# Kernel tuning notes

Measured on AMD Instinct MI355X. Metric: run time of the kernel, lower is better.

The kernel has to match this reference:

```python
import jax, jax.numpy as jnp
import numpy as np

HIDDEN = 4096
INTER = 11008
B, S = 8, 16
QMAX = 127  # int8 symmetric range for w_bits=8


def setup_inputs() -> dict:
    key = jax.random.key(0)
    ks = jax.random.split(key, 7)
    hidden_state = jax.random.normal(ks[0], (B, S, HIDDEN), dtype=jnp.float32)
    # Quantized weights stored as integer values in float32 (as the dequant source)
    w1_q = jax.random.randint(ks[1], (INTER, HIDDEN), -QMAX - 1, QMAX + 1).astype(jnp.float32)
    w3_q = jax.random.randint(ks[2], (INTER, HIDDEN), -QMAX - 1, QMAX + 1).astype(jnp.float32)
    w2_q = jax.random.randint(ks[3], (HIDDEN, INTER), -QMAX - 1, QMAX + 1).astype(jnp.float32)
    # Per-output-channel dequant scales (has_scale=True)
    w1_s = jax.random.uniform(ks[4], (INTER,), dtype=jnp.float32, minval=0.5, maxval=1.5) * 0.01
    w3_s = jax.random.uniform(ks[5], (INTER,), dtype=jnp.float32, minval=0.5, maxval=1.5) * 0.01
    w2_s = jax.random.uniform(ks[6], (HIDDEN,), dtype=jnp.float32, minval=0.5, maxval=1.5) * 0.01
    return {"hidden_state": hidden_state, "w1_q": w1_q, "w1_s": w1_s,
            "w3_q": w3_q, "w3_s": w3_s, "w2_q": w2_q, "w2_s": w2_s}


def _dequant_linear(x, w_q, w_s):
    # w_q: [out, in] integer-valued weights; w_s: [out] per-channel scale
    # y = x @ (w_q * w_s[:, None]).T == (x @ w_q.T) * w_s
    return jnp.einsum('bsh,oh->bso', x, w_q) * w_s


def reference(hidden_state, w1_q, w1_s, w3_q, w3_s, w2_q, w2_s):
    up = _dequant_linear(hidden_state, w1_q, w1_s)      # [B,S,INTER]
    gate = _dequant_linear(hidden_state, w3_q, w3_s)    # [B,S,INTER]
    h = jax.nn.silu(up) * gate                          # SwiGLU
    return _dequant_linear(h, w2_q, w2_s)               # [B,S,HIDDEN]
```

## Files before the change

kernel.cpp:

```cpp
#include <hip/hip_runtime.h>

#define HIDDEN 4096
#define INTER  11008
#define MTOK   128
#define NMERG  (2*INTER)
#define KS1    4
#define KS2    16

typedef short          short8  __attribute__((ext_vector_type(8)));
typedef unsigned short ushort8 __attribute__((ext_vector_type(8)));
typedef float          f32x16  __attribute__((ext_vector_type(16)));
#define AS1 __attribute__((address_space(1)))
#define AS3 __attribute__((address_space(3)))

static __device__ __forceinline__ unsigned short f2bf_rne(float f) {
    unsigned u = __builtin_bit_cast(unsigned, f);
    u += 0x7FFFu + ((u >> 16) & 1u);
    return (unsigned short)(u >> 16);
}
static __device__ __forceinline__ float bf2f(unsigned short b) {
    unsigned u = (unsigned)b << 16;
    return __builtin_bit_cast(float, u);
}
static __device__ __forceinline__ int pk2(float lo, float hi) {
    return (int)__builtin_amdgcn_perm(__builtin_bit_cast(unsigned, hi),
                                      __builtin_bit_cast(unsigned, lo),
                                      0x07060302u);
}

__global__ void cvt_x_k(const float* __restrict__ x, unsigned short* __restrict__ A2) {
    int f = blockIdx.x * 256 + threadIdx.x;
    int lane = f & 63, w = f >> 6;
    int kstep = w >> 2, ms = w & 3;
    int m = ms * 32 + (lane & 31);
    int k = kstep * 16 + (lane >> 5) * 8;
    const float* src = x + (size_t)m * HIDDEN + k;
    float4 v0 = *(const float4*)(src);
    float4 v1 = *(const float4*)(src + 4);
    ushort8 o;
    o[0] = f2bf_rne(v0.x); o[1] = f2bf_rne(v0.y); o[2] = f2bf_rne(v0.z); o[3] = f2bf_rne(v0.w);
    o[4] = f2bf_rne(v1.x); o[5] = f2bf_rne(v1.y); o[6] = f2bf_rne(v1.z); o[7] = f2bf_rne(v1.w);
    *(ushort8*)(A2 + (size_t)f * 8) = o;
}

template<bool OBF16>
__global__ __launch_bounds__(256) void gemm_k(
    const unsigned short* __restrict__ A2,
    const float* __restrict__ B0, const float* __restrict__ B1, int nhalf,
    void* __restrict__ part, int K, int N, int totTiles, int ksplit)
{
    __shared__ __align__(16) float lds[16384];
    const int lane = threadIdx.x & 63;
    const int ws   = threadIdx.x >> 6;
    const int n0   = blockIdx.x * 128;
    const int ks   = blockIdx.y;
    const int tbeg = (ks * totTiles) / ksplit;
    const int tend = ((ks + 1) * totTiles) / ksplit;
    const int nt   = tend - tbeg;

    const char* gbase[8];
#pragma unroll
    for (int i = 0; i < 8; ++i) {
        int s = ws * 512 + i * 64 + lane;
        int n = s >> 4;
        int a = (s & 15) ^ (n & 15);
        const float* rowp = (n0 + n < nhalf) ? (B0 + (size_t)(n0 + n) * K)
                                             : (B1 + (size_t)(n0 + n - nhalf) * K);
        gbase[i] = (const char*)rowp + a * 16;
    }

    f32x16 acc[4];
#pragma unroll
    for (int t = 0; t < 4; ++t)
#pragma unroll
        for (int r = 0; r < 16; ++r) acc[t][r] = 0.f;

    const int nl = ws * 32 + (lane & 31);

    auto stage = [&](int t, int buf) {
        const size_t koff = (size_t)t * 64 * 4;
#pragma unroll
        for (int i = 0; i < 8; ++i) {
            __builtin_amdgcn_global_load_lds(
                (const AS1 unsigned*)(gbase[i] + koff),
                (AS3 unsigned*)((char*)lds + buf * 32768 + ws * 8192 + i * 1024), 16, 0, 0);
        }
    };
    auto loadA = [&](int t, short8 (&Ar)[16]) {
#pragma unroll
        for (int r = 0; r < 16; ++r) {
            int kg = t * 4 + (r >> 2), ms = r & 3;
            Ar[r] = *(const short8*)(A2 + ((size_t)(kg * 4 + ms) * 64 + lane) * 8);
        }
    };

    short8 A0[16], A1[16];

    auto iter = [&](int i, short8 (&Ar)[16]) {
        if (i + 1 < nt) { asm volatile("s_waitcnt vmcnt(24)" ::: "memory"); }
        else            { asm volatile("s_waitcnt vmcnt(0)" ::: "memory"); }
        __builtin_amdgcn_sched_barrier(0);

        const char* lbase = (const char*)lds + (size_t)(i & 1) * 32768;
#pragma unroll
        for (int step = 0; step < 4; ++step) {
            int a0 = step * 4 + ((lane >> 5) << 1);
            int p0 = nl * 16 + (a0 ^ (nl & 15));
            int p1 = nl * 16 + ((a0 + 1) ^ (nl & 15));
            float4 v0 = *(const float4*)(lbase + p0 * 16);
            float4 v1 = *(const float4*)(lbase + p1 * 16);
            int4 bi;
            bi.x = pk2(v0.x, v0.y); bi.y = pk2(v0.z, v0.w);
            bi.z = pk2(v1.x, v1.y); bi.w = pk2(v1.z, v1.w);
            short8 bf = __builtin_bit_cast(short8, bi);
#pragma unroll
            for (int ms = 0; ms < 4; ++ms)
                acc[ms] = __builtin_amdgcn_mfma_f32_32x32x16_bf16(Ar[step * 4 + ms], bf, acc[ms], 0, 0, 0);
        }

        if (i + 2 < nt) {
            asm volatile("s_waitcnt lgkmcnt(0)" ::: "memory");
            __builtin_amdgcn_sched_barrier(0);
            stage(tbeg + i + 2, i & 1);
            loadA(tbeg + i + 2, Ar);
        }
    };

    stage(tbeg, 0);
    loadA(tbeg, A0);
    if (nt > 1) { stage(tbeg + 1, 1); loadA(tbeg + 1, A1); }

    for (int i = 0; i < nt; i += 2) {
        iter(i, A0);
        if (i + 1 < nt) iter(i + 1, A1);
    }

    const int n = n0 + ws * 32 + (lane & 31);
#pragma unroll
    for (int ms = 0; ms < 4; ++ms)
#pragma unroll
        for (int r = 0; r < 16; ++r) {
            int m = ms * 32 + (r & 3) + 8 * (r >> 2) + 4 * (lane >> 5);
            size_t idx = ((size_t)ks * MTOK + m) * (size_t)N + n;
            if (OBF16) ((unsigned short*)part)[idx] = f2bf_rne(acc[ms][r]);
            else       ((float*)part)[idx] = acc[ms][r];
        }
}

__global__ void swiglu_k(const unsigned short* __restrict__ p1,
                         const float* __restrict__ s1, const float* __restrict__ s3,
                         unsigned short* __restrict__ h2)
{
    int f = blockIdx.x * 256 + threadIdx.x;
    int lane = f & 63, w = f >> 6;
    int kstep = w >> 2, ms = w & 3;
    int m = ms * 32 + (lane & 31);
    int j = kstep * 16 + (lane >> 5) * 8;
    float up[8], gt[8];
#pragma unroll
    for (int e = 0; e < 8; ++e) { up[e] = 0.f; gt[e] = 0.f; }
#pragma unroll
    for (int ks = 0; ks < KS1; ++ks) {
        const unsigned short* pu = p1 + ((size_t)ks * MTOK + m) * NMERG + j;
        ushort8 u = *(const ushort8*)(pu);
        ushort8 g = *(const ushort8*)(pu + INTER);
#pragma unroll
        for (int e = 0; e < 8; ++e) { up[e] += bf2f(u[e]); gt[e] += bf2f(g[e]); }
    }
    float4 c1a = *(const float4*)(s1 + j), c1b = *(const float4*)(s1 + j + 4);
    float4 c3a = *(const float4*)(s3 + j), c3b = *(const float4*)(s3 + j + 4);
    float c1[8] = {c1a.x, c1a.y, c1a.z, c1a.w, c1b.x, c1b.y, c1b.z, c1b.w};
    float c3[8] = {c3a.x, c3a.y, c3a.z, c3a.w, c3b.x, c3b.y, c3b.z, c3b.w};
    ushort8 o;
#pragma unroll
    for (int e = 0; e < 8; ++e) {
        float u = up[e] * c1[e], g = gt[e] * c3[e];
        o[e] = f2bf_rne(g * u / (1.f + __expf(-u)));
    }
    *(ushort8*)(h2 + (size_t)f * 8) = o;
}

__global__ void reduce_k(const float* __restrict__ p, const float* __restrict__ s2,
                         float* __restrict__ out)
{
    int i = (blockIdx.x * 256 + threadIdx.x) * 4;
    float4 acc = *(const float4*)(p + i);
#pragma unroll
    for (int s = 1; s < KS2; ++s) {
        float4 v = *(const float4*)(p + (size_t)s * MTOK * HIDDEN + i);
        acc.x += v.x; acc.y += v.y; acc.z += v.z; acc.w += v.w;
    }
    int ncol = i & (HIDDEN - 1);
    float4 sc = *(const float4*)(s2 + ncol);
    acc.x *= sc.x; acc.y *= sc.y; acc.z *= sc.z; acc.w *= sc.w;
    *(float4*)(out + i) = acc;
}

extern "C" void kernel_launch(void* const* d_in, const int* in_sizes, int n_in,
                              void* d_out, int out_size, void* d_ws, size_t ws_size,
                              hipStream_t stream) {
    const float* x   = (const float*)d_in[0];
    const float* w1q = (const float*)d_in[1];
    const float* w1s = (const float*)d_in[2];
    const float* w3q = (const float*)d_in[3];
    const float* w3s = (const float*)d_in[4];
    const float* w2q = (const float*)d_in[5];
    const float* w2s = (const float*)d_in[6];
    float* out = (float*)d_out;

    char* ws = (char*)d_ws;
    unsigned short* xb2 = (unsigned short*)ws;
    unsigned short* h2  = (unsigned short*)(ws + (1u << 20));
    void* part          = (void*)(ws + (4u << 20));

    cvt_x_k<<<MTOK * HIDDEN / 8 / 256, 256, 0, stream>>>(x, xb2);
    gemm_k<true><<<dim3(NMERG / 128, KS1), 256, 0, stream>>>(
        xb2, w1q, w3q, INTER, part, HIDDEN, NMERG, HIDDEN / 64, KS1);
    swiglu_k<<<MTOK * INTER / 8 / 256, 256, 0, stream>>>(
        (const unsigned short*)part, w1s, w3s, h2);
    gemm_k<false><<<dim3(HIDDEN / 128, KS2), 256, 0, stream>>>(
        h2, w2q, w2q, 1 << 30, part, INTER, HIDDEN, INTER / 64, KS2);
    reduce_k<<<MTOK * HIDDEN / 4 / 256, 256, 0, stream>>>(
        (const float*)part, w2s, out);
}
```

Before: 528.9 us.

## Retile GEMM to 32-column N tiles with 256-deep K stages and less split-K

Shrinks each block's output tile from 128 to 32 weight rows, with each wave owning one 32-token M slice instead of an N slice. Each stage now loads 256 K values per row into padded LDS rows. Split-K drops from 4/16 to 1/4, so there are far fewer partial-sum writes and reads while the grid grows in N. Block-wide barriers are added around LDS reuse. The cost is that each B fragment now feeds only one MFMA per wave, and the K loop per block is longer.

```diff
diff --git a/kernel.cpp b/kernel.cpp
--- a/kernel.cpp
+++ b/kernel.cpp
@@ -4,8 +4,11 @@
 #define INTER  11008
 #define MTOK   128
 #define NMERG  (2*INTER)
-#define KS1    4
-#define KS2    16
+#define KS1    1
+#define KS2    4
+#define SK     256
+#define RST    1040
+#define TILE   (32*RST)
 
 typedef short          short8  __attribute__((ext_vector_type(8)));
 typedef unsigned short ushort8 __attribute__((ext_vector_type(8)));
@@ -49,102 +52,88 @@
     const float* __restrict__ B0, const float* __restrict__ B1, int nhalf,
     void* __restrict__ part, int K, int N, int totTiles, int ksplit)
 {
-    __shared__ __align__(16) float lds[16384];
+    __shared__ __align__(16) char lds[2 * TILE];
     const int lane = threadIdx.x & 63;
     const int ws   = threadIdx.x >> 6;
-    const int n0   = blockIdx.x * 128;
+    const int n0   = blockIdx.x * 32;
     const int ks   = blockIdx.y;
     const int tbeg = (ks * totTiles) / ksplit;
     const int tend = ((ks + 1) * totTiles) / ksplit;
     const int nt   = tend - tbeg;
 
-    const char* gbase[8];
-#pragma unroll
-    for (int i = 0; i < 8; ++i) {
-        int s = ws * 512 + i * 64 + lane;
-        int n = s >> 4;
-        int a = (s & 15) ^ (n & 15);
-        const float* rowp = (n0 + n < nhalf) ? (B0 + (size_t)(n0 + n) * K)
-                                             : (B1 + (size_t)(n0 + n - nhalf) * K);
-        gbase[i] = (const char*)rowp + a * 16;
-    }
-
-    f32x16 acc[4];
-#pragma unroll
-    for (int t = 0; t < 4; ++t)
-#pragma unroll
-        for (int r = 0; r < 16; ++r) acc[t][r] = 0.f;
-
-    const int nl = ws * 32 + (lane & 31);
+    const char* rowp[8];
+#pragma unroll
+    for (int r = 0; r < 8; ++r) {
+        int n = n0 + ws * 8 + r;
+        const float* p = (n < nhalf) ? B0 + (size_t)n * K
+                                     : B1 + (size_t)(n - nhalf) * K;
+        rowp[r] = (const char*)p + lane * 16;
+    }
+
+    f32x16 acc;
+#pragma unroll
+    for (int r = 0; r < 16; ++r) acc[r] = 0.f;
 
     auto stage = [&](int t, int buf) {
-        const size_t koff = (size_t)t * 64 * 4;
-#pragma unroll
-        for (int i = 0; i < 8; ++i) {
+        const size_t koff = (size_t)t * (SK * 4);
+#pragma unroll
+        for (int r = 0; r < 8; ++r) {
             __builtin_amdgcn_global_load_lds(
-                (const AS1 unsigned*)(gbase[i] + koff),
-                (AS3 unsigned*)((char*)lds + buf * 32768 + ws * 8192 + i * 1024), 16, 0, 0);
+                (const AS1 unsigned*)(rowp[r] + koff),
+                (AS3 unsigned*)(lds + buf * TILE + (ws * 8 + r) * RST), 16, 0, 0);
         }
     };
     auto loadA = [&](int t, short8 (&Ar)[16]) {
 #pragma unroll
-        for (int r = 0; r < 16; ++r) {
-            int kg = t * 4 + (r >> 2), ms = r & 3;
-            Ar[r] = *(const short8*)(A2 + ((size_t)(kg * 4 + ms) * 64 + lane) * 8);
+        for (int s = 0; s < 16; ++s) {
+            int kg = t * 16 + s;
+            Ar[s] = *(const short8*)(A2 + ((size_t)(kg * 4 + ws) * 64 + lane) * 8);
         }
     };
 
-    short8 A0[16], A1[16];
+    short8 A0v[16], A1v[16];
 
     auto iter = [&](int i, short8 (&Ar)[16]) {
         if (i + 1 < nt) { asm volatile("s_waitcnt vmcnt(24)" ::: "memory"); }
-        else            { asm volatile("s_waitcnt vmcnt(0)" ::: "memory"); }
+        else            { asm volatile("s_waitcnt vmcnt(0)"  ::: "memory"); }
         __builtin_amdgcn_sched_barrier(0);
-
-        const char* lbase = (const char*)lds + (size_t)(i & 1) * 32768;
-#pragma unroll
-        for (int step = 0; step < 4; ++step) {
-            int a0 = step * 4 + ((lane >> 5) << 1);
-            int p0 = nl * 16 + (a0 ^ (nl & 15));
-            int p1 = nl * 16 + ((a0 + 1) ^ (nl & 15));
-            float4 v0 = *(const float4*)(lbase + p0 * 16);
-            float4 v1 = *(const float4*)(lbase + p1 * 16);
+        __builtin_amdgcn_s_barrier();
+
+        const char* lb = lds + (size_t)(i & 1) * TILE
+                       + (lane & 31) * RST + (lane >> 5) * 32;
+#pragma unroll
+        for (int s = 0; s < 16; ++s) {
+            float4 v0 = *(const float4*)(lb + s * 64);
+            float4 v1 = *(const float4*)(lb + s * 64 + 16);
             int4 bi;
             bi.x = pk2(v0.x, v0.y); bi.y = pk2(v0.z, v0.w);
             bi.z = pk2(v1.x, v1.y); bi.w = pk2(v1.z, v1.w);
             short8 bf = __builtin_bit_cast(short8, bi);
-#pragma unroll
-            for (int ms = 0; ms < 4; ++ms)
-                acc[ms] = __builtin_amdgcn_mfma_f32_32x32x16_bf16(Ar[step * 4 + ms], bf, acc[ms], 0, 0, 0);
+            acc = __builtin_amdgcn_mfma_f32_32x32x16_bf16(Ar[s], bf, acc, 0, 0, 0);
         }
 
-        if (i + 2 < nt) {
-            asm volatile("s_waitcnt lgkmcnt(0)" ::: "memory");
-            __builtin_amdgcn_sched_barrier(0);
-            stage(tbeg + i + 2, i & 1);
-            loadA(tbeg + i + 2, Ar);
-        }
+        asm volatile("s_waitcnt lgkmcnt(0)" ::: "memory");
+        __builtin_amdgcn_sched_barrier(0);
+        __builtin_amdgcn_s_barrier();
+        if (i + 2 < nt) { stage(tbeg + i + 2, i & 1); loadA(tbeg + i + 2, Ar); }
     };
 
-    stage(tbeg, 0);
-    loadA(tbeg, A0);
-    if (nt > 1) { stage(tbeg + 1, 1); loadA(tbeg + 1, A1); }
+    stage(tbeg, 0); loadA(tbeg, A0v);
+    if (nt > 1) { stage(tbeg + 1, 1); loadA(tbeg + 1, A1v); }
 
     for (int i = 0; i < nt; i += 2) {
-        iter(i, A0);
-        if (i + 1 < nt) iter(i + 1, A1);
-    }
-
-    const int n = n0 + ws * 32 + (lane & 31);
-#pragma unroll
-    for (int ms = 0; ms < 4; ++ms)
-#pragma unroll
-        for (int r = 0; r < 16; ++r) {
-            int m = ms * 32 + (r & 3) + 8 * (r >> 2) + 4 * (lane >> 5);
-            size_t idx = ((size_t)ks * MTOK + m) * (size_t)N + n;
-            if (OBF16) ((unsigned short*)part)[idx] = f2bf_rne(acc[ms][r]);
-            else       ((float*)part)[idx] = acc[ms][r];
-        }
+        iter(i, A0v);
+        if (i + 1 < nt) iter(i + 1, A1v);
+    }
+
+    const int n = n0 + (lane & 31);
+#pragma unroll
+    for (int r = 0; r < 16; ++r) {
+        int m = ws * 32 + (r & 3) + 8 * (r >> 2) + 4 * (lane >> 5);
+        size_t idx = ((size_t)ks * MTOK + m) * (size_t)N + n;
+        if (OBF16) ((unsigned short*)part)[idx] = f2bf_rne(acc[r]);
+        else       ((float*)part)[idx] = acc[r];
+    }
 }
 
 __global__ void swiglu_k(const unsigned short* __restrict__ p1,
@@ -214,12 +203,12 @@
     void* part          = (void*)(ws + (4u << 20));
 
     cvt_x_k<<<MTOK * HIDDEN / 8 / 256, 256, 0, stream>>>(x, xb2);
-    gemm_k<true><<<dim3(NMERG / 128, KS1), 256, 0, stream>>>(
-        xb2, w1q, w3q, INTER, part, HIDDEN, NMERG, HIDDEN / 64, KS1);
+    gemm_k<true><<<dim3(NMERG / 32, KS1), 256, 0, stream>>>(
+        xb2, w1q, w3q, INTER, part, HIDDEN, NMERG, HIDDEN / SK, KS1);
     swiglu_k<<<MTOK * INTER / 8 / 256, 256, 0, stream>>>(
         (const unsigned short*)part, w1s, w3s, h2);
-    gemm_k<false><<<dim3(HIDDEN / 128, KS2), 256, 0, stream>>>(
-        h2, w2q, w2q, 1 << 30, part, INTER, HIDDEN, INTER / 64, KS2);
+    gemm_k<false><<<dim3(HIDDEN / 32, KS2), 256, 0, stream>>>(
+        h2, w2q, w2q, 1 << 30, part, INTER, HIDDEN, INTER / SK, KS2);
     reduce_k<<<MTOK * HIDDEN / 4 / 256, 256, 0, stream>>>(
         (const float*)part, w2s, out);
 }
```

After: 513.7 us. -2.9%, faster.
